# Optimization experiments

Hardware: AMD Instinct MI355X
Metric: run time of the kernel (lower is better)

The kernel has to match this reference:

```python
import jax, jax.numpy as jnp
import numpy as np

B, C, H, W = 8, 256, 128, 128
CQK = C // 16


def setup_inputs() -> dict:
    key = jax.random.key(0)
    ks = jax.random.split(key, 8)
    x = jax.random.normal(ks[0], (B, C, H, W), dtype=jnp.float32)
    # 1x1 convs == channel matmuls; store weights as [out_ch, in_ch]
    sc = 1.0 / np.sqrt(C)
    Wq = jax.random.normal(ks[1], (CQK, C), dtype=jnp.float32) * sc
    bq = jax.random.normal(ks[2], (CQK,), dtype=jnp.float32) * 0.01
    Wk = jax.random.normal(ks[3], (CQK, C), dtype=jnp.float32) * sc
    bk = jax.random.normal(ks[4], (CQK,), dtype=jnp.float32) * 0.01
    Wv = jax.random.normal(ks[5], (C, C), dtype=jnp.float32) * sc
    bv = jax.random.normal(ks[6], (C,), dtype=jnp.float32) * 0.01
    # gamma initialized to zero in the torch module; use a nonzero value so the
    # attention path actually contributes to the output being checked.
    gamma = jnp.full((1,), 0.5, dtype=jnp.float32)
    return {"x": x, "Wq": Wq, "bq": bq, "Wk": Wk, "bk": bk,
            "Wv": Wv, "bv": bv, "gamma": gamma}


def reference(x, Wq, bq, Wk, bk, Wv, bv, gamma):
    b, c, h, w = x.shape
    hw = h * w
    if hw > 4096:
        s = int((hw / 4096) ** 0.5)  # static python int (shapes are static)
        hd, wd = h // s, w // s
        # avg_pool2d kernel=stride=s
        xd = x.reshape(b, c, hd, s, wd, s).mean(axis=(3, 5))
    else:
        xd, hd, wd = x, h, w
    n = hd * wd
    # 1x1 conv projections as channel contractions
    q = (jnp.einsum('oc,bchw->bohw', Wq, xd) + bq[None, :, None, None]).reshape(b, -1, n)  # [b,d,n]
    k = (jnp.einsum('oc,bchw->bohw', Wk, xd) + bk[None, :, None, None]).reshape(b, -1, n)  # [b,d,n]
    v = (jnp.einsum('oc,bchw->bohw', Wv, xd) + bv[None, :, None, None]).reshape(b, c, n)   # [b,c,n]
    # attention[b,n,m] = softmax_m( q[:,n]^T k[:,m] )
    scores = jnp.einsum('bdn,bdm->bnm', q, k)
    attn = jax.nn.softmax(scores, axis=-1)
    # out[b,c,n] = sum_m v[b,c,m] * attn[b,n,m]  (bmm(value, attn^T))
    out = jnp.einsum('bcm,bnm->bcn', v, attn).reshape(b, c, hd, wd)
    if (hd, wd) != (h, w):
        # bilinear, align_corners=False (half-pixel) == jax.image.resize bilinear
        out = jax.image.resize(out, (b, c, h, w), method='bilinear')
    return gamma * out + x
```

## Files before the change

### kernel.cpp

```cpp
#include <hip/hip_runtime.h>

typedef short bf16x8 __attribute__((ext_vector_type(8)));
typedef short bf16x4 __attribute__((ext_vector_type(4)));
typedef float f32x16 __attribute__((ext_vector_type(16)));
typedef int i32x4 __attribute__((ext_vector_type(4)));
typedef unsigned short ushort_t;

#define MFMA32(a, b, c) __builtin_amdgcn_mfma_f32_32x32x16_bf16(a, b, c, 0, 0, 0)
#define LOG2E 1.4426950408889634f

__device__ __forceinline__ unsigned short f2b(float f) {
  unsigned u = __float_as_uint(f);
  u += 0x7fffu + ((u >> 16) & 1u);
  return (unsigned short)(u >> 16);
}
__device__ __forceinline__ float b2f(unsigned short v) {
  return __uint_as_float(((unsigned)v) << 16);
}
__device__ __forceinline__ f32x16 zero16() {
  f32x16 z;
#pragma unroll
  for (int i = 0; i < 16; ++i) z[i] = 0.0f;
  return z;
}
__device__ __forceinline__ int cvtpk(float lo, float hi) {
  int r;
  asm("v_cvt_pk_bf16_f32 %0, %1, %2" : "=v"(r) : "v"(lo), "v"(hi));
  return r;
}

#define WS_XD 0u
#define WS_QT 16777216u
#define WS_KT 17825792u
#define WS_OBF 18874368u
#define WS_OP 35651584u
#define WS_WVB 52428800u

__global__ void k_down(const float* __restrict__ x, ushort_t* __restrict__ xd) {
  int i = blockIdx.x * 256 + threadIdx.x;
  int wx = i & 63, hy = (i >> 6) & 63, cb = i >> 12;
  const float* p = x + (size_t)cb * 16384;
  float2 a = *(const float2*)(p + (2 * hy) * 128 + 2 * wx);
  float2 b = *(const float2*)(p + (2 * hy + 1) * 128 + 2 * wx);
  xd[i] = f2b((a.x + a.y + b.x + b.y) * 0.25f);
}

__global__ void k_wvb(const float* __restrict__ Wv, ushort_t* __restrict__ Wvb) {
  int i = blockIdx.x * 256 + threadIdx.x;
  Wvb[i] = f2b(Wv[i]);
}

__global__ __launch_bounds__(256) void k_projqk(
    const ushort_t* __restrict__ xd, const float* __restrict__ Wq,
    const float* __restrict__ bq, const float* __restrict__ Wk,
    const float* __restrict__ bk, ushort_t* __restrict__ QT,
    ushort_t* __restrict__ KT) {
  __shared__ float Wsh[2][256][16];
  int t = threadIdx.x;
#pragma unroll
  for (int i = 0; i < 16; ++i) {
    int e = t + 256 * i;
    int d = e & 15, c = e >> 4;
    Wsh[0][c][d] = Wq[d * 256 + c];
    Wsh[1][c][d] = Wk[d * 256 + c];
  }
  __syncthreads();
  int b = blockIdx.x >> 6, nt = blockIdx.x & 63;
  int w = t >> 6, n = nt * 64 + (t & 63);
  const ushort_t* xr = xd + (size_t)b * 1048576 + n;
  float qa0 = bq[4 * w], qa1 = bq[4 * w + 1], qa2 = bq[4 * w + 2], qa3 = bq[4 * w + 3];
  float ka0 = bk[4 * w], ka1 = bk[4 * w + 1], ka2 = bk[4 * w + 2], ka3 = bk[4 * w + 3];
#pragma unroll 4
  for (int c = 0; c < 256; ++c) {
    float xv = b2f(xr[(size_t)c * 4096]);
    float4 wq = *(const float4*)(&Wsh[0][c][4 * w]);
    float4 wk = *(const float4*)(&Wsh[1][c][4 * w]);
    qa0 += wq.x * xv; qa1 += wq.y * xv; qa2 += wq.z * xv; qa3 += wq.w * xv;
    ka0 += wk.x * xv; ka1 += wk.y * xv; ka2 += wk.z * xv; ka3 += wk.w * xv;
  }
  size_t o = (((size_t)b * 4096 + n) << 4) + 4 * w;
  bf16x4 qv, kv;
  qv[0] = (short)f2b(qa0 * LOG2E); qv[1] = (short)f2b(qa1 * LOG2E);
  qv[2] = (short)f2b(qa2 * LOG2E); qv[3] = (short)f2b(qa3 * LOG2E);
  kv[0] = (short)f2b(ka0); kv[1] = (short)f2b(ka1); kv[2] = (short)f2b(ka2); kv[3] = (short)f2b(ka3);
  *(bf16x4*)(QT + o) = qv;
  *(bf16x4*)(KT + o) = kv;
}

__global__ __launch_bounds__(512, 2) void k_attn(
    const ushort_t* __restrict__ xd, const ushort_t* __restrict__ QT,
    const ushort_t* __restrict__ KT, ushort_t* __restrict__ Obf) {
  __shared__ __align__(16) char smem[65536];
  const int t = threadIdx.x;
  const int b = blockIdx.x >> 5;
  const int n0 = (blockIdx.x & 31) * 128;
  const int w = t >> 6, lane = t & 63, lq = lane & 31, g = lane >> 5;
  const int qg = w >> 2, cg = w & 3;

  bf16x8 qf0 = *(const bf16x8*)(QT + (((size_t)b * 4096 + n0 + 64 * qg + lq) << 4) + 8 * g);
  bf16x8 qf1 = *(const bf16x8*)(QT + (((size_t)b * 4096 + n0 + 64 * qg + 32 + lq) << 4) + 8 * g);
  const size_t kbase = (size_t)b * 65536;

  float sm0 = 0.f, sm1 = 0.f;
  f32x16 acc00 = zero16(), acc01 = zero16(), acc10 = zero16(), acc11 = zero16();
  const ushort_t* vsrc = xd + (size_t)b * 1048576;
  const int srow = t >> 3, mch = t & 7;

#pragma unroll
  for (int i = 0; i < 4; ++i) {
    int c = srow + 64 * i;
    bf16x8 v = *(const bf16x8*)(vsrc + (size_t)c * 4096 + 8 * mch);
    int base = c * 128, sw = (c & 15) << 3;
    *(bf16x4*)(&smem[base + ((16 * mch) ^ sw)]) = __builtin_shufflevector(v, v, 0, 1, 2, 3);
    *(bf16x4*)(&smem[base + ((16 * mch + 8) ^ sw)]) = __builtin_shufflevector(v, v, 4, 5, 6, 7);
  }
  __syncthreads();
  int cur = 0;
  for (int mt = 0; mt < 64; ++mt) {
    bf16x8 stg[4];
    if (mt < 63) {
      int m0n = (mt + 1) * 64;
#pragma unroll
      for (int i = 0; i < 4; ++i) {
        int c = srow + 64 * i;
        stg[i] = *(const bf16x8*)(vsrc + (size_t)c * 4096 + m0n + 8 * mch);
      }
    }
    bf16x8 pf0[4], pf1[4];
#pragma unroll
    for (int ms = 0; ms < 2; ++ms) {
      int m = mt * 64 + 32 * ms + lq;
      bf16x8 kf = *(const bf16x8*)(KT + kbase + ((size_t)m << 4) + 8 * g);
      f32x16 s0 = MFMA32(kf, qf0, zero16());
      f32x16 s1 = MFMA32(kf, qf1, zero16());
      float p0[16], p1[16];
#pragma unroll
      for (int r = 0; r < 16; ++r) {
        p0[r] = exp2f(s0[r]); sm0 += p0[r];
        p1[r] = exp2f(s1[r]); sm1 += p1[r];
      }
#pragma unroll
      for (int h = 0; h < 2; ++h) {
        i32x4 w0, w1;
#pragma unroll
        for (int pr = 0; pr < 4; ++pr) {
          w0[pr] = cvtpk(p0[8 * h + 2 * pr], p0[8 * h + 2 * pr + 1]);
          w1[pr] = cvtpk(p1[8 * h + 2 * pr], p1[8 * h + 2 * pr + 1]);
        }
        pf0[2 * ms + h] = __builtin_bit_cast(bf16x8, w0);
        pf1[2 * ms + h] = __builtin_bit_cast(bf16x8, w1);
      }
    }
    {
      int cbase = 64 * cg + lq;
      int bufb = cur * 32768;
#pragma unroll
      for (int kk = 0; kk < 4; ++kk) {
#pragma unroll
        for (int jt = 0; jt < 2; ++jt) {
          int c = cbase + 32 * jt;
          int rb = bufb + c * 128, sw = (c & 15) << 3;
          bf16x4 u0 = *(const bf16x4*)(&smem[rb + ((32 * kk + 8 * g) ^ sw)]);
          bf16x4 u1 = *(const bf16x4*)(&smem[rb + ((32 * kk + 8 * g + 16) ^ sw)]);
          bf16x8 vb = __builtin_shufflevector(u0, u1, 0, 1, 2, 3, 4, 5, 6, 7);
          if (jt == 0) {
            acc00 = MFMA32(pf0[kk], vb, acc00);
            acc10 = MFMA32(pf1[kk], vb, acc10);
          } else {
            acc01 = MFMA32(pf0[kk], vb, acc01);
            acc11 = MFMA32(pf1[kk], vb, acc11);
          }
        }
      }
    }
    if (mt < 63) {
      int nb = (cur ^ 1) * 32768;
#pragma unroll
      for (int i = 0; i < 4; ++i) {
        int c = srow + 64 * i;
        int base = nb + c * 128, sw = (c & 15) << 3;
        *(bf16x4*)(&smem[base + ((16 * mch) ^ sw)]) = __builtin_shufflevector(stg[i], stg[i], 0, 1, 2, 3);
        *(bf16x4*)(&smem[base + ((16 * mch + 8) ^ sw)]) = __builtin_shufflevector(stg[i], stg[i], 4, 5, 6, 7);
      }
    }
    __syncthreads();
    cur ^= 1;
  }
  sm0 += __shfl_xor(sm0, 32);
  sm1 += __shfl_xor(sm1, 32);
  float inv0 = 1.0f / sm0, inv1 = 1.0f / sm1;
  size_t obase = (size_t)b * 1048576;
  int c0 = 64 * cg + lq, c1 = c0 + 32;
#pragma unroll
  for (int r = 0; r < 16; ++r) {
    int q32 = (r & 3) + 8 * (r >> 2) + 4 * g;
    float sc0 = __shfl(inv0, q32);
    float sc1 = __shfl(inv1, q32);
    int n = n0 + 64 * qg + q32;
    size_t row0 = obase + (size_t)n * 256;
    size_t row1 = obase + (size_t)(n + 32) * 256;
    Obf[row0 + c0] = f2b(acc00[r] * sc0);
    Obf[row0 + c1] = f2b(acc01[r] * sc0);
    Obf[row1 + c0] = f2b(acc10[r] * sc1);
    Obf[row1 + c1] = f2b(acc11[r] * sc1);
  }
}

__global__ __launch_bounds__(256) void k_gemmv(const ushort_t* __restrict__ Obf,
                                               const ushort_t* __restrict__ Wvb,
                                               const float* __restrict__ bv,
                                               ushort_t* __restrict__ OP) {
  int t = threadIdx.x;
  int b = blockIdx.x >> 6, nt = blockIdx.x & 63;
  int n0 = nt * 64;
  int w = t >> 6, lane = t & 63, lq = lane & 31, g = lane >> 5;
  f32x16 a00 = zero16(), a01 = zero16(), a10 = zero16(), a11 = zero16();
  const ushort_t* arow0 = Obf + ((size_t)b * 4096 + n0 + lq) * 256 + 8 * g;
  const ushort_t* arow1 = arow0 + 32 * 256;
  const ushort_t* brow0 = Wvb + (size_t)(64 * w + lq) * 256 + 8 * g;
  const ushort_t* brow1 = brow0 + 32 * 256;
#pragma unroll 4
  for (int kk = 0; kk < 16; ++kk) {
    bf16x8 A0 = *(const bf16x8*)(arow0 + 16 * kk);
    bf16x8 A1 = *(const bf16x8*)(arow1 + 16 * kk);
    bf16x8 B0 = *(const bf16x8*)(brow0 + 16 * kk);
    bf16x8 B1 = *(const bf16x8*)(brow1 + 16 * kk);
    a00 = MFMA32(A0, B0, a00);
    a01 = MFMA32(A0, B1, a01);
    a10 = MFMA32(A1, B0, a10);
    a11 = MFMA32(A1, B1, a11);
  }
#pragma unroll
  for (int cs = 0; cs < 2; ++cs) {
    int cout = 64 * w + 32 * cs + lq;
    float bias = bv[cout];
    size_t cb = ((size_t)b * 256 + cout) * 4096 + n0;
#pragma unroll
    for (int r = 0; r < 16; ++r) {
      int nl = (r & 3) + 8 * (r >> 2) + 4 * g;
      if (cs == 0) {
        OP[cb + nl] = f2b(a00[r] + bias);
        OP[cb + 32 + nl] = f2b(a10[r] + bias);
      } else {
        OP[cb + nl] = f2b(a01[r] + bias);
        OP[cb + 32 + nl] = f2b(a11[r] + bias);
      }
    }
  }
}

__global__ void k_up(const ushort_t* __restrict__ OP, const float* __restrict__ x,
                     const float* __restrict__ gamma, float* __restrict__ out) {
  int i = blockIdx.x * 256 + threadIdx.x;
  int xq = i & 31, y = (i >> 5) & 127, cb = i >> 12;
  float gm = gamma[0];
  int iy0 = (y - 1) >> 1;
  float wy = (y & 1) ? 0.25f : 0.75f;
  int iy1 = min(iy0 + 1, 63);
  iy0 = max(iy0, 0);
  const ushort_t* prow = OP + (size_t)cb * 4096;
  const ushort_t* r0 = prow + iy0 * 64;
  const ushort_t* r1 = prow + iy1 * 64;
  float v[4];
#pragma unroll
  for (int j = 0; j < 4; ++j) {
    int xx = xq * 4 + j;
    int ix0 = (xx - 1) >> 1;
    float wx = (xx & 1) ? 0.25f : 0.75f;
    int ix1 = min(ix0 + 1, 63);
    ix0 = max(ix0, 0);
    float o00 = b2f(r0[ix0]), o01 = b2f(r0[ix1]);
    float o10 = b2f(r1[ix0]), o11 = b2f(r1[ix1]);
    float top = o00 + wx * (o01 - o00);
    float bot = o10 + wx * (o11 - o10);
    v[j] = top + wy * (bot - top);
  }
  size_t o = ((size_t)cb * 128 + y) * 128 + xq * 4;
  float4 xv = *(const float4*)(x + o);
  float4 ov;
  ov.x = gm * v[0] + xv.x;
  ov.y = gm * v[1] + xv.y;
  ov.z = gm * v[2] + xv.z;
  ov.w = gm * v[3] + xv.w;
  *(float4*)(out + o) = ov;
}

extern "C" void kernel_launch(void* const* d_in, const int* in_sizes, int n_in,
                              void* d_out, int out_size, void* d_ws, size_t ws_size,
                              hipStream_t stream) {
  const float* x = (const float*)d_in[0];
  const float* Wq = (const float*)d_in[1];
  const float* bq = (const float*)d_in[2];
  const float* Wk = (const float*)d_in[3];
  const float* bk = (const float*)d_in[4];
  const float* Wv = (const float*)d_in[5];
  const float* bv = (const float*)d_in[6];
  const float* gamma = (const float*)d_in[7];
  char* ws = (char*)d_ws;
  ushort_t* xd = (ushort_t*)(ws + WS_XD);
  ushort_t* QT = (ushort_t*)(ws + WS_QT);
  ushort_t* KT = (ushort_t*)(ws + WS_KT);
  ushort_t* Obf = (ushort_t*)(ws + WS_OBF);
  ushort_t* OP = (ushort_t*)(ws + WS_OP);
  ushort_t* Wvb = (ushort_t*)(ws + WS_WVB);
  float* outp = (float*)d_out;

  k_down<<<32768, 256, 0, stream>>>(x, xd);
  k_wvb<<<256, 256, 0, stream>>>(Wv, Wvb);
  k_projqk<<<512, 256, 0, stream>>>(xd, Wq, bq, Wk, bk, QT, KT);
  k_attn<<<256, 512, 0, stream>>>(xd, QT, KT, Obf);
  k_gemmv<<<512, 256, 0, stream>>>(Obf, Wvb, bv, OP);
  k_up<<<32768, 256, 0, stream>>>(OP, x, gamma, outp);
}
```

Baseline: 533.4 us.

## Halve attention query tile per block and compute softmax row sums with MFMA

```diff
diff --git a/kernel.cpp b/kernel.cpp
--- a/kernel.cpp
+++ b/kernel.cpp
@@ -27,6 +27,15 @@
   int r;
   asm("v_cvt_pk_bf16_f32 %0, %1, %2" : "=v"(r) : "v"(lo), "v"(hi));
   return r;
+}
+__device__ __forceinline__ float fexp2(float x) {
+#if __has_builtin(__builtin_amdgcn_exp2f)
+  return __builtin_amdgcn_exp2f(x);
+#else
+  float r;
+  asm("v_exp_f32 %0, %1" : "=v"(r) : "v"(x));
+  return r;
+#endif
 }
 
 #define WS_XD 0u
@@ -87,122 +96,117 @@
   *(bf16x4*)(KT + o) = kv;
 }
 
-__global__ __launch_bounds__(512, 2) void k_attn(
+__global__ __launch_bounds__(512, 4) void k_attn(
     const ushort_t* __restrict__ xd, const ushort_t* __restrict__ QT,
     const ushort_t* __restrict__ KT, ushort_t* __restrict__ Obf) {
   __shared__ __align__(16) char smem[65536];
   const int t = threadIdx.x;
-  const int b = blockIdx.x >> 5;
-  const int n0 = (blockIdx.x & 31) * 128;
+  const int b = blockIdx.x >> 6;
+  const int n0 = (blockIdx.x & 63) * 64;
   const int w = t >> 6, lane = t & 63, lq = lane & 31, g = lane >> 5;
   const int qg = w >> 2, cg = w & 3;
 
-  bf16x8 qf0 = *(const bf16x8*)(QT + (((size_t)b * 4096 + n0 + 64 * qg + lq) << 4) + 8 * g);
-  bf16x8 qf1 = *(const bf16x8*)(QT + (((size_t)b * 4096 + n0 + 64 * qg + 32 + lq) << 4) + 8 * g);
-  const size_t kbase = (size_t)b * 65536;
-
-  float sm0 = 0.f, sm1 = 0.f;
-  f32x16 acc00 = zero16(), acc01 = zero16(), acc10 = zero16(), acc11 = zero16();
+  bf16x8 qf0 = *(const bf16x8*)(QT + (((size_t)b * 4096 + n0 + 32 * qg + lq) << 4) + 8 * g);
+
+  bf16x8 ones;
+#pragma unroll
+  for (int e = 0; e < 8; ++e) ones[e] = (short)0x3F80;
+
+  f32x16 acc0 = zero16(), acc1 = zero16(), accs = zero16();
+
   const ushort_t* vsrc = xd + (size_t)b * 1048576;
   const int srow = t >> 3, mch = t & 7;
+  const int wsw = (srow & 15) << 3;
+  const int wb0 = srow * 128 + ((16 * mch) ^ wsw);
+  const int wb1 = srow * 128 + ((16 * mch + 8) ^ wsw);
+  const int rsw = (lq & 15) << 3;
+  const int cb0 = (64 * cg + lq) * 128;
+  const int cb1 = cb0 + 4096;
+  int Doff[4][2];
+#pragma unroll
+  for (int kk = 0; kk < 4; ++kk)
+#pragma unroll
+    for (int h = 0; h < 2; ++h)
+      Doff[kk][h] = ((32 * kk) ^ (rsw & 0x60)) + ((16 * h) ^ (rsw & 0x10)) + ((8 * g) ^ (rsw & 0x08));
+
+  const ushort_t* kp = KT + (size_t)b * 65536 + (lq << 4) + 8 * g;
+  const ushort_t* vp = vsrc + (size_t)srow * 4096 + 8 * mch;
 
 #pragma unroll
   for (int i = 0; i < 4; ++i) {
-    int c = srow + 64 * i;
-    bf16x8 v = *(const bf16x8*)(vsrc + (size_t)c * 4096 + 8 * mch);
-    int base = c * 128, sw = (c & 15) << 3;
-    *(bf16x4*)(&smem[base + ((16 * mch) ^ sw)]) = __builtin_shufflevector(v, v, 0, 1, 2, 3);
-    *(bf16x4*)(&smem[base + ((16 * mch + 8) ^ sw)]) = __builtin_shufflevector(v, v, 4, 5, 6, 7);
+    bf16x8 v = *(const bf16x8*)(vp + (size_t)i * 262144);
+    *(bf16x4*)(&smem[wb0 + 8192 * i]) = __builtin_shufflevector(v, v, 0, 1, 2, 3);
+    *(bf16x4*)(&smem[wb1 + 8192 * i]) = __builtin_shufflevector(v, v, 4, 5, 6, 7);
   }
   __syncthreads();
   int cur = 0;
   for (int mt = 0; mt < 64; ++mt) {
     bf16x8 stg[4];
     if (mt < 63) {
-      int m0n = (mt + 1) * 64;
-#pragma unroll
-      for (int i = 0; i < 4; ++i) {
-        int c = srow + 64 * i;
-        stg[i] = *(const bf16x8*)(vsrc + (size_t)c * 4096 + m0n + 8 * mch);
+      const ushort_t* vn = vp + (mt + 1) * 64;
+#pragma unroll
+      for (int i = 0; i < 4; ++i) stg[i] = *(const bf16x8*)(vn + (size_t)i * 262144);
+    }
+    bf16x8 kf0 = *(const bf16x8*)(kp);
+    bf16x8 kf1 = *(const bf16x8*)(kp + 512);
+    kp += 1024;
+    f32x16 s0 = MFMA32(kf0, qf0, zero16());
+    f32x16 s1 = MFMA32(kf1, qf0, zero16());
+    bf16x8 pf[4];
+#pragma unroll
+    for (int q = 0; q < 4; ++q) {
+      i32x4 wv;
+#pragma unroll
+      for (int pr = 0; pr < 4; ++pr) {
+        float a, c;
+        if (q < 2) {
+          a = fexp2(s0[8 * (q & 1) + 2 * pr]);
+          c = fexp2(s0[8 * (q & 1) + 2 * pr + 1]);
+        } else {
+          a = fexp2(s1[8 * (q & 1) + 2 * pr]);
+          c = fexp2(s1[8 * (q & 1) + 2 * pr + 1]);
+        }
+        wv[pr] = cvtpk(a, c);
       }
-    }
-    bf16x8 pf0[4], pf1[4];
-#pragma unroll
-    for (int ms = 0; ms < 2; ++ms) {
-      int m = mt * 64 + 32 * ms + lq;
-      bf16x8 kf = *(const bf16x8*)(KT + kbase + ((size_t)m << 4) + 8 * g);
-      f32x16 s0 = MFMA32(kf, qf0, zero16());
-      f32x16 s1 = MFMA32(kf, qf1, zero16());
-      float p0[16], p1[16];
-#pragma unroll
-      for (int r = 0; r < 16; ++r) {
-        p0[r] = exp2f(s0[r]); sm0 += p0[r];
-        p1[r] = exp2f(s1[r]); sm1 += p1[r];
-      }
-#pragma unroll
-      for (int h = 0; h < 2; ++h) {
-        i32x4 w0, w1;
-#pragma unroll
-        for (int pr = 0; pr < 4; ++pr) {
-          w0[pr] = cvtpk(p0[8 * h + 2 * pr], p0[8 * h + 2 * pr + 1]);
-          w1[pr] = cvtpk(p1[8 * h + 2 * pr], p1[8 * h + 2 * pr + 1]);
-        }
-        pf0[2 * ms + h] = __builtin_bit_cast(bf16x8, w0);
-        pf1[2 * ms + h] = __builtin_bit_cast(bf16x8, w1);
-      }
+      pf[q] = __builtin_bit_cast(bf16x8, wv);
     }
     {
-      int cbase = 64 * cg + lq;
-      int bufb = cur * 32768;
+      int a0 = cb0 + cur * 32768;
+      int a1 = cb1 + cur * 32768;
 #pragma unroll
       for (int kk = 0; kk < 4; ++kk) {
-#pragma unroll
-        for (int jt = 0; jt < 2; ++jt) {
-          int c = cbase + 32 * jt;
-          int rb = bufb + c * 128, sw = (c & 15) << 3;
-          bf16x4 u0 = *(const bf16x4*)(&smem[rb + ((32 * kk + 8 * g) ^ sw)]);
-          bf16x4 u1 = *(const bf16x4*)(&smem[rb + ((32 * kk + 8 * g + 16) ^ sw)]);
-          bf16x8 vb = __builtin_shufflevector(u0, u1, 0, 1, 2, 3, 4, 5, 6, 7);
-          if (jt == 0) {
-            acc00 = MFMA32(pf0[kk], vb, acc00);
-            acc10 = MFMA32(pf1[kk], vb, acc10);
-          } else {
-            acc01 = MFMA32(pf0[kk], vb, acc01);
-            acc11 = MFMA32(pf1[kk], vb, acc11);
-          }
-        }
+        bf16x4 u0 = *(const bf16x4*)(&smem[a0 + Doff[kk][0]]);
+        bf16x4 u1 = *(const bf16x4*)(&smem[a0 + Doff[kk][1]]);
+        bf16x8 vb = __builtin_shufflevector(u0, u1, 0, 1, 2, 3, 4, 5, 6, 7);
+        acc0 = MFMA32(pf[kk], vb, acc0);
+        bf16x4 u2 = *(const bf16x4*)(&smem[a1 + Doff[kk][0]]);
+        bf16x4 u3 = *(const bf16x4*)(&smem[a1 + Doff[kk][1]]);
+        bf16x8 vc = __builtin_shufflevector(u2, u3, 0, 1, 2, 3, 4, 5, 6, 7);
+        acc1 = MFMA32(pf[kk], vc, acc1);
+        accs = MFMA32(pf[kk], ones, accs);
       }
     }
     if (mt < 63) {
       int nb = (cur ^ 1) * 32768;
 #pragma unroll
       for (int i = 0; i < 4; ++i) {
-        int c = srow + 64 * i;
-        int base = nb + c * 128, sw = (c & 15) << 3;
-        *(bf16x4*)(&smem[base + ((16 * mch) ^ sw)]) = __builtin_shufflevector(stg[i], stg[i], 0, 1, 2, 3);
-        *(bf16x4*)(&smem[base + ((16 * mch + 8) ^ sw)]) = __builtin_shufflevector(stg[i], stg[i], 4, 5, 6, 7);
+        *(bf16x4*)(&smem[wb0 + nb + 8192 * i]) = __builtin_shufflevector(stg[i], stg[i], 0, 1, 2, 3);
+        *(bf16x4*)(&smem[wb1 + nb + 8192 * i]) = __builtin_shufflevector(stg[i], stg[i], 4, 5, 6, 7);
       }
     }
     __syncthreads();
     cur ^= 1;
   }
-  sm0 += __shfl_xor(sm0, 32);
-  sm1 += __shfl_xor(sm1, 32);
-  float inv0 = 1.0f / sm0, inv1 = 1.0f / sm1;
   size_t obase = (size_t)b * 1048576;
   int c0 = 64 * cg + lq, c1 = c0 + 32;
 #pragma unroll
   for (int r = 0; r < 16; ++r) {
     int q32 = (r & 3) + 8 * (r >> 2) + 4 * g;
-    float sc0 = __shfl(inv0, q32);
-    float sc1 = __shfl(inv1, q32);
-    int n = n0 + 64 * qg + q32;
-    size_t row0 = obase + (size_t)n * 256;
-    size_t row1 = obase + (size_t)(n + 32) * 256;
-    Obf[row0 + c0] = f2b(acc00[r] * sc0);
-    Obf[row0 + c1] = f2b(acc01[r] * sc0);
-    Obf[row1 + c0] = f2b(acc10[r] * sc1);
-    Obf[row1 + c1] = f2b(acc11[r] * sc1);
+    float inv = 1.0f / accs[r];
+    int n = n0 + 32 * qg + q32;
+    size_t row = obase + (size_t)n * 256;
+    Obf[row + c0] = f2b(acc0[r] * inv);
+    Obf[row + c1] = f2b(acc1[r] * inv);
   }
 }
 
@@ -308,7 +312,7 @@
   k_down<<<32768, 256, 0, stream>>>(x, xd);
   k_wvb<<<256, 256, 0, stream>>>(Wv, Wvb);
   k_projqk<<<512, 256, 0, stream>>>(xd, Wq, bq, Wk, bk, QT, KT);
-  k_attn<<<256, 512, 0, stream>>>(xd, QT, KT, Obf);
+  k_attn<<<512, 512, 0, stream>>>(xd, QT, KT, Obf);
   k_gemmv<<<512, 256, 0, stream>>>(Obf, Wvb, bv, OP);
   k_up<<<32768, 256, 0, stream>>>(OP, x, gamma, outp);
 }
```

Measured after the change: 460.7 us. 1.16x faster.
